# Optimization experiments

Measured on AMD Instinct MI355X. Metric: run time of the kernel, lower is better.

## Reference

```python
import jax, jax.numpy as jnp
import numpy as np

BSZ, T, D_IN, P, H, D_OUT = 8, 4096, 512, 256, 256, 512


def setup_inputs() -> dict:
    key = jax.random.key(0)
    ks = jax.random.split(key, 8)
    x_seq = jax.random.normal(ks[0], (BSZ, T, D_IN), dtype=jnp.float32)
    # stable diagonal transition: |a| < 1 so the 4096-step recurrence does not blow up
    a = jax.random.uniform(ks[1], (H,), minval=-0.99, maxval=0.99, dtype=jnp.float32)
    B = jax.random.normal(ks[2], (P, H), dtype=jnp.float32) * 0.05
    C = jax.random.normal(ks[3], (H, P), dtype=jnp.float32) * 0.05
    Wi = jax.random.normal(ks[4], (P, D_IN), dtype=jnp.float32) * 0.05
    bi = jax.random.normal(ks[5], (P,), dtype=jnp.float32) * 0.05
    Wo = jax.random.normal(ks[6], (D_OUT, P), dtype=jnp.float32) * 0.05
    bo = jax.random.normal(ks[7], (D_OUT,), dtype=jnp.float32) * 0.05
    return {"x_seq": x_seq, "a": a, "B": B, "C": C, "Wi": Wi, "bi": bi, "Wo": Wo, "bo": bo}


def reference(x_seq, a, B, C, Wi, bi, Wo, bo):
    # proj_in + relu (eqx.nn.Linear: y = W @ x + b), vmapped over batch and time
    x_proj = jax.nn.relu(jnp.einsum("btd,pd->btp", x_seq, Wi) + bi)  # [Bsz,T,P]
    # precompute driving input u_t = B^T x_t for every step
    u = jnp.einsum("btp,ph->bth", x_proj, B)  # [Bsz,T,H]
    u_t = jnp.swapaxes(u, 0, 1)  # [T,Bsz,H] (scan over time)

    def step(h, u_step):  # h: [Bsz,H]
        h = a * h + u_step
        return h, h

    h0 = jnp.zeros((x_seq.shape[0], a.shape[0]), dtype=x_seq.dtype)
    _, hs = jax.lax.scan(step, h0, u_t)  # hs: [T,Bsz,H]
    # y_t = C^T h_t, then proj_out
    y_seq = jnp.einsum("tbh,hp->btp", hs, C)  # [Bsz,T,P]
    y_out = jnp.einsum("btp,op->bto", y_seq, Wo) + bo  # [Bsz,T,D_out]
    return y_out
```

## Files before the change

kernel.cpp:

```cpp
#include <hip/hip_runtime.h>

#define BSZN 8
#define TT 4096
#define DIN 512
#define PP 256
#define HHH 256
#define DOUT 512
#define NROWS (BSZN * TT)
#define LCH 128
#define NC (TT / LCH)

typedef __attribute__((ext_vector_type(8))) short bf16x8;
typedef __attribute__((ext_vector_type(4))) float f32x4;

#define GLOBAL_AS __attribute__((address_space(1)))
#define LDS_AS __attribute__((address_space(3)))

static __device__ __forceinline__ void gld_lds16(const void* g, void* l) {
  __builtin_amdgcn_global_load_lds((const GLOBAL_AS unsigned int*)g,
                                   (LDS_AS unsigned int*)l, 16, 0, 0);
}

static __device__ __forceinline__ unsigned short f2bf(float x) {
  union { float f; unsigned u; } t{x};
  unsigned r = t.u + 0x7fffu + ((t.u >> 16) & 1u);
  return (unsigned short)(r >> 16);
}

__global__ __launch_bounds__(256) void gemm_cwt(
    const unsigned short* __restrict__ Ap, const unsigned short* __restrict__ Bp,
    unsigned short* __restrict__ Cp, int M, int N, int K) {
  __shared__ alignas(16) char smem[16384];
  char* As = smem;
  char* Bs = smem + 8192;
  const int tid = threadIdx.x, wave = tid >> 6, lane = tid & 63;
  const int m0 = blockIdx.x * 128, n0 = blockIdx.y * 128;
  const int wrow = (wave >> 1) * 64, wcol = (wave & 1) * 64;

  f32x4 acc[4][4];
#pragma unroll
  for (int i = 0; i < 4; ++i)
#pragma unroll
    for (int j = 0; j < 4; ++j) acc[i][j] = f32x4{0.f, 0.f, 0.f, 0.f};

  for (int k0 = 0; k0 < K; k0 += 32) {
#pragma unroll
    for (int it = 0; it < 2; ++it) {
      const int r = it * 64 + wave * 16 + (lane >> 2);
      const int cB = (lane & 3) * 16;
      gld_lds16((const char*)(Ap + (size_t)(m0 + r) * K + k0) + cB, As + r * 64 + cB);
      gld_lds16((const char*)(Bp + (size_t)(n0 + r) * K + k0) + cB, Bs + r * 64 + cB);
    }
    __syncthreads();
    bf16x8 af[4], bfv[4];
#pragma unroll
    for (int mi = 0; mi < 4; ++mi)
      af[mi] = *(const bf16x8*)(As + (wrow + mi * 16 + (lane & 15)) * 64 + (lane >> 4) * 16);
#pragma unroll
    for (int ni = 0; ni < 4; ++ni)
      bfv[ni] = *(const bf16x8*)(Bs + (wcol + ni * 16 + (lane & 15)) * 64 + (lane >> 4) * 16);
#pragma unroll
    for (int mi = 0; mi < 4; ++mi)
#pragma unroll
      for (int ni = 0; ni < 4; ++ni)
        acc[mi][ni] = __builtin_amdgcn_mfma_f32_16x16x32_bf16(af[mi], bfv[ni], acc[mi][ni], 0, 0, 0);
    __syncthreads();
  }
#pragma unroll
  for (int mi = 0; mi < 4; ++mi)
#pragma unroll
    for (int ni = 0; ni < 4; ++ni)
#pragma unroll
      for (int reg = 0; reg < 4; ++reg) {
        const int row = m0 + wrow + mi * 16 + (lane >> 4) * 4 + reg;
        const int col = n0 + wcol + ni * 16 + (lane & 15);
        Cp[(size_t)row * N + col] = f2bf(acc[mi][ni][reg]);
      }
}

__global__ __launch_bounds__(256) void conv_w_k(
    const float* __restrict__ Wi, const float* __restrict__ Wo,
    const float* __restrict__ Cm, const float* __restrict__ Bm,
    unsigned short* __restrict__ Wi_b, unsigned short* __restrict__ Wo_b,
    unsigned short* __restrict__ C_b, unsigned short* __restrict__ B_bT,
    int* __restrict__ flag_g) {
  const int b = blockIdx.x;
  const int tid = threadIdx.x;
  if (b < 320) {
    const float* src;
    unsigned short* dst;
    int idx;
    if (b < 128) { src = Wi; dst = Wi_b; idx = b * 1024 + tid * 4; }
    else if (b < 256) { src = Wo; dst = Wo_b; idx = (b - 128) * 1024 + tid * 4; }
    else { src = Cm; dst = C_b; idx = (b - 256) * 1024 + tid * 4; }
    const float4 v = *(const float4*)(src + idx);
    uint2 w;
    w.x = (unsigned)f2bf(v.x) | ((unsigned)f2bf(v.y) << 16);
    w.y = (unsigned)f2bf(v.z) | ((unsigned)f2bf(v.w) << 16);
    *(uint2*)(dst + idx) = w;
  } else if (b < 576) {
    const int p = b - 320;
    const int h = tid;
    B_bT[(size_t)h * PP + p] = f2bf(Bm[(size_t)p * HHH + h]);
  } else {
    flag_g[tid] = 0;
  }
}

__global__ __launch_bounds__(256, 1) void s4_mega(
    const float* __restrict__ x, const float* __restrict__ a,
    const unsigned short* __restrict__ Wi_b, const float* __restrict__ bi,
    const unsigned short* __restrict__ B_bT,
    const unsigned short* __restrict__ CWT_b, const float* __restrict__ bo,
    float* __restrict__ out, float* __restrict__ carry_g,
    int* __restrict__ flag_g) {
  __shared__ alignas(16) char smem[65536];
  char* As = smem;
  char* Bs = smem + 8192;

  const int tid = threadIdx.x, wave = tid >> 6, lane = tid & 63;
  const int bc = blockIdx.x, b = bc >> 5, c = bc & 31;
  const size_t row0 = (size_t)bc * LCH;
  const int wrow = (wave >> 1) * 64;
  const int wcol = (wave & 1) * 128;
  const int l15 = lane & 15, q = lane >> 4;

  f32x4 acc[4][8];
#pragma unroll
  for (int i = 0; i < 4; ++i)
#pragma unroll
    for (int j = 0; j < 8; ++j) acc[i][j] = f32x4{0.f, 0.f, 0.f, 0.f};

  for (int k0 = 0; k0 < DIN; k0 += 32) {
#pragma unroll
    for (int it = 0; it < 4; ++it) {
      const int f = it * 256 + tid;
      const int r = f >> 3, ck = (f & 7) * 4;
      const float4 v = *(const float4*)(x + (row0 + r) * DIN + k0 + ck);
      uint2 w;
      w.x = (unsigned)f2bf(v.x) | ((unsigned)f2bf(v.y) << 16);
      w.y = (unsigned)f2bf(v.z) | ((unsigned)f2bf(v.w) << 16);
      *(uint2*)(As + r * 64 + ck * 2) = w;
    }
#pragma unroll
    for (int it = 0; it < 4; ++it) {
      const int R0 = it * 64 + wave * 16;
      const int row = R0 + (lane >> 2), cB = (lane & 3) * 16;
      gld_lds16((const char*)(Wi_b + (size_t)row * DIN + k0) + cB, Bs + row * 64 + cB);
    }
    __syncthreads();
    bf16x8 af[4], bfv[8];
#pragma unroll
    for (int mi = 0; mi < 4; ++mi)
      af[mi] = *(const bf16x8*)(As + (wrow + mi * 16 + l15) * 64 + q * 16);
#pragma unroll
    for (int ni = 0; ni < 8; ++ni)
      bfv[ni] = *(const bf16x8*)(Bs + (wcol + ni * 16 + l15) * 64 + q * 16);
#pragma unroll
    for (int mi = 0; mi < 4; ++mi)
#pragma unroll
      for (int ni = 0; ni < 8; ++ni)
        acc[mi][ni] = __builtin_amdgcn_mfma_f32_16x16x32_bf16(af[mi], bfv[ni], acc[mi][ni], 0, 0, 0);
    __syncthreads();
  }

  unsigned short* xp = (unsigned short*)smem;
#pragma unroll
  for (int mi = 0; mi < 4; ++mi)
#pragma unroll
    for (int ni = 0; ni < 8; ++ni) {
      const int col = wcol + ni * 16 + l15;
      const float bb = bi[col];
#pragma unroll
      for (int reg = 0; reg < 4; ++reg) {
        const int row = wrow + mi * 16 + q * 4 + reg;
        float v = acc[mi][ni][reg] + bb;
        v = fmaxf(v, 0.f);
        xp[row * 256 + col] = f2bf(v);
      }
    }
  __syncthreads();

  f32x4 uacc[4][8];
#pragma unroll
  for (int i = 0; i < 4; ++i)
#pragma unroll
    for (int j = 0; j < 8; ++j) uacc[i][j] = f32x4{0.f, 0.f, 0.f, 0.f};
  for (int k0 = 0; k0 < PP; k0 += 32) {
    bf16x8 af[4], bfv[8];
#pragma unroll
    for (int mi = 0; mi < 4; ++mi)
      af[mi] = *(const bf16x8*)(xp + (wrow + mi * 16 + l15) * 256 + k0 + q * 8);
#pragma unroll
    for (int ni = 0; ni < 8; ++ni) {
      const int h = wcol + ni * 16 + l15;
      bfv[ni] = *(const bf16x8*)(B_bT + (size_t)h * PP + k0 + q * 8);
    }
#pragma unroll
    for (int mi = 0; mi < 4; ++mi)
#pragma unroll
      for (int ni = 0; ni < 8; ++ni)
        uacc[mi][ni] = __builtin_amdgcn_mfma_f32_16x16x32_bf16(af[mi], bfv[ni], uacc[mi][ni], 0, 0, 0);
  }
  __syncthreads();

  float carry0 = 0.f, carry1 = 0.f;
  float* uL = (float*)smem;
#pragma unroll
  for (int kh = 0; kh < 2; ++kh) {
    if ((wave & 1) == kh) {
#pragma unroll
      for (int mi = 0; mi < 4; ++mi)
#pragma unroll
        for (int ni = 0; ni < 8; ++ni) {
          const int colh = ni * 16 + l15;
#pragma unroll
          for (int reg = 0; reg < 4; ++reg) {
            const int row = wrow + mi * 16 + q * 4 + reg;
            uL[row * 128 + colh] = uacc[mi][ni][reg];
          }
        }
    }
    __syncthreads();
    if (tid < 128) {
      const float ah = a[kh * 128 + tid];
      float l = 0.f;
#pragma unroll 4
      for (int i = 0; i < LCH; ++i) {
        l = fmaf(ah, l, uL[i * 128 + tid]);
        uL[i * 128 + tid] = l;
      }
      if (kh == 0) carry0 = l; else carry1 = l;
    }
    __syncthreads();
    if ((wave & 1) == kh) {
#pragma unroll
      for (int mi = 0; mi < 4; ++mi)
#pragma unroll
        for (int ni = 0; ni < 8; ++ni) {
          const int colh = ni * 16 + l15;
#pragma unroll
          for (int reg = 0; reg < 4; ++reg) {
            const int row = wrow + mi * 16 + q * 4 + reg;
            uacc[mi][ni][reg] = uL[row * 128 + colh];
          }
        }
    }
    __syncthreads();
  }

  if (tid < 128) {
    __hip_atomic_store(&carry_g[(size_t)bc * HHH + tid], carry0,
                       __ATOMIC_RELAXED, __HIP_MEMORY_SCOPE_AGENT);
    __hip_atomic_store(&carry_g[(size_t)bc * HHH + 128 + tid], carry1,
                       __ATOMIC_RELAXED, __HIP_MEMORY_SCOPE_AGENT);
  }
  __syncthreads();
  if (tid == 0) {
    __threadfence();
    __hip_atomic_store(&flag_g[bc], 1, __ATOMIC_RELEASE, __HIP_MEMORY_SCOPE_AGENT);
  }
  if (tid < c) {
    while (__hip_atomic_load(&flag_g[b * NC + tid], __ATOMIC_ACQUIRE,
                             __HIP_MEMORY_SCOPE_AGENT) == 0)
      __builtin_amdgcn_s_sleep(8);
  }
  __syncthreads();
  float P = 0.f;
  {
    const float ah = a[tid];
    float aL = ah;
#pragma unroll
    for (int j = 0; j < 7; ++j) aL *= aL;
    for (int j = 0; j < c; ++j)
      P = fmaf(aL, P,
               __hip_atomic_load(&carry_g[((size_t)b * NC + j) * HHH + tid],
                                 __ATOMIC_RELAXED, __HIP_MEMORY_SCOPE_AGENT));
  }
  float* PL = (float*)smem;
  PL[tid] = P;
  __syncthreads();
#pragma unroll
  for (int ni = 0; ni < 8; ++ni) {
    const int col = wcol + ni * 16 + l15;
    const float Pc = PL[col];
    const float A = a[col];
    const float A2 = A * A, A4 = A2 * A2, A8 = A4 * A4, A16 = A8 * A8;
    const float A32 = A16 * A16, A64 = A32 * A32;
    float base = A * ((q & 1) ? A4 : 1.f) * ((q & 2) ? A8 : 1.f) *
                 (wrow ? A64 : 1.f);
    float rowf = base;
#pragma unroll
    for (int mi = 0; mi < 4; ++mi) {
      float fr = rowf;
#pragma unroll
      for (int reg = 0; reg < 4; ++reg) {
        uacc[mi][ni][reg] = fmaf(fr, Pc, uacc[mi][ni][reg]);
        fr *= A;
      }
      rowf *= A16;
    }
  }
  __syncthreads();

  unsigned short* hsL = (unsigned short*)smem;
#pragma unroll
  for (int mi = 0; mi < 4; ++mi)
#pragma unroll
    for (int ni = 0; ni < 8; ++ni) {
      const int col = wcol + ni * 16 + l15;
#pragma unroll
      for (int reg = 0; reg < 4; ++reg) {
        const int row = wrow + mi * 16 + q * 4 + reg;
        hsL[row * 256 + col] = f2bf(uacc[mi][ni][reg]);
      }
    }
  __syncthreads();

  for (int n = 0; n < 4; ++n) {
    f32x4 oacc[4][4];
#pragma unroll
    for (int i = 0; i < 4; ++i)
#pragma unroll
      for (int j = 0; j < 4; ++j) oacc[i][j] = f32x4{0.f, 0.f, 0.f, 0.f};
    const int ocol0 = n * 128 + (wave & 1) * 64;
    for (int k0 = 0; k0 < HHH; k0 += 32) {
      bf16x8 af[4], bfv[4];
#pragma unroll
      for (int mi = 0; mi < 4; ++mi)
        af[mi] = *(const bf16x8*)(hsL + (wrow + mi * 16 + l15) * 256 + k0 + q * 8);
#pragma unroll
      for (int ni = 0; ni < 4; ++ni) {
        const int o = ocol0 + ni * 16 + l15;
        bfv[ni] = *(const bf16x8*)(CWT_b + (size_t)o * HHH + k0 + q * 8);
      }
#pragma unroll
      for (int mi = 0; mi < 4; ++mi)
#pragma unroll
        for (int ni = 0; ni < 4; ++ni)
          oacc[mi][ni] = __builtin_amdgcn_mfma_f32_16x16x32_bf16(af[mi], bfv[ni], oacc[mi][ni], 0, 0, 0);
    }
#pragma unroll
    for (int ni = 0; ni < 4; ++ni) {
      const int o = ocol0 + ni * 16 + l15;
      const float bb = bo[o];
#pragma unroll
      for (int mi = 0; mi < 4; ++mi)
#pragma unroll
        for (int reg = 0; reg < 4; ++reg) {
          const int row = wrow + mi * 16 + q * 4 + reg;
          out[(row0 + row) * DOUT + o] = oacc[mi][ni][reg] + bb;
        }
    }
  }
}

extern "C" void kernel_launch(void* const* d_in, const int* in_sizes, int n_in,
                              void* d_out, int out_size, void* d_ws,
                              size_t ws_size, hipStream_t stream) {
  const float* x  = (const float*)d_in[0];
  const float* a  = (const float*)d_in[1];
  const float* Bm = (const float*)d_in[2];
  const float* Cm = (const float*)d_in[3];
  const float* Wi = (const float*)d_in[4];
  const float* bi = (const float*)d_in[5];
  const float* Wo = (const float*)d_in[6];
  const float* bo = (const float*)d_in[7];
  float* out = (float*)d_out;

  char* ws = (char*)d_ws;
  unsigned short* Wi_b  = (unsigned short*)ws; ws += (size_t)PP * DIN * 2;
  unsigned short* Wo_b  = (unsigned short*)ws; ws += (size_t)DOUT * PP * 2;
  unsigned short* C_b   = (unsigned short*)ws; ws += (size_t)HHH * PP * 2;
  unsigned short* B_bT  = (unsigned short*)ws; ws += (size_t)HHH * PP * 2;
  unsigned short* CWT_b = (unsigned short*)ws; ws += (size_t)DOUT * HHH * 2;
  float* carry_g = (float*)ws; ws += (size_t)BSZN * NC * HHH * 4;
  int* flag_g = (int*)ws;

  conv_w_k<<<577, 256, 0, stream>>>(Wi, Wo, Cm, Bm, Wi_b, Wo_b, C_b, B_bT, flag_g);
  gemm_cwt<<<dim3(DOUT / 128, HHH / 128), 256, 0, stream>>>(Wo_b, C_b, CWT_b,
                                                            DOUT, HHH, PP);
  s4_mega<<<BSZN * NC, 256, 0, stream>>>(x, a, Wi_b, bi, B_bT, CWT_b, bo, out,
                                         carry_g, flag_g);
}
```

Measured before the change: 196.3 us.

## Halve chunk length, do in-register scan, merge prep kernels, raise occupancy

```diff
diff --git a/kernel.cpp b/kernel.cpp
--- a/kernel.cpp
+++ b/kernel.cpp
@@ -6,9 +6,10 @@
 #define PP 256
 #define HHH 256
 #define DOUT 512
-#define NROWS (BSZN * TT)
-#define LCH 128
-#define NC (TT / LCH)
+#define LCH 64
+#define NCH (TT / LCH)
+#define NBLK (BSZN * NCH)
+#define XPS 264
 
 typedef __attribute__((ext_vector_type(8))) short bf16x8;
 typedef __attribute__((ext_vector_type(4))) float f32x4;
@@ -27,233 +28,236 @@
   return (unsigned short)(r >> 16);
 }
 
-__global__ __launch_bounds__(256) void gemm_cwt(
-    const unsigned short* __restrict__ Ap, const unsigned short* __restrict__ Bp,
-    unsigned short* __restrict__ Cp, int M, int N, int K) {
-  __shared__ alignas(16) char smem[16384];
-  char* As = smem;
-  char* Bs = smem + 8192;
-  const int tid = threadIdx.x, wave = tid >> 6, lane = tid & 63;
-  const int m0 = blockIdx.x * 128, n0 = blockIdx.y * 128;
-  const int wrow = (wave >> 1) * 64, wcol = (wave & 1) * 64;
-
-  f32x4 acc[4][4];
-#pragma unroll
-  for (int i = 0; i < 4; ++i)
-#pragma unroll
-    for (int j = 0; j < 4; ++j) acc[i][j] = f32x4{0.f, 0.f, 0.f, 0.f};
-
-  for (int k0 = 0; k0 < K; k0 += 32) {
-#pragma unroll
-    for (int it = 0; it < 2; ++it) {
-      const int r = it * 64 + wave * 16 + (lane >> 2);
-      const int cB = (lane & 3) * 16;
-      gld_lds16((const char*)(Ap + (size_t)(m0 + r) * K + k0) + cB, As + r * 64 + cB);
-      gld_lds16((const char*)(Bp + (size_t)(n0 + r) * K + k0) + cB, Bs + r * 64 + cB);
-    }
-    __syncthreads();
-    bf16x8 af[4], bfv[4];
-#pragma unroll
-    for (int mi = 0; mi < 4; ++mi)
-      af[mi] = *(const bf16x8*)(As + (wrow + mi * 16 + (lane & 15)) * 64 + (lane >> 4) * 16);
-#pragma unroll
-    for (int ni = 0; ni < 4; ++ni)
-      bfv[ni] = *(const bf16x8*)(Bs + (wcol + ni * 16 + (lane & 15)) * 64 + (lane >> 4) * 16);
-#pragma unroll
-    for (int mi = 0; mi < 4; ++mi)
-#pragma unroll
-      for (int ni = 0; ni < 4; ++ni)
-        acc[mi][ni] = __builtin_amdgcn_mfma_f32_16x16x32_bf16(af[mi], bfv[ni], acc[mi][ni], 0, 0, 0);
-    __syncthreads();
-  }
-#pragma unroll
-  for (int mi = 0; mi < 4; ++mi)
-#pragma unroll
-    for (int ni = 0; ni < 4; ++ni)
-#pragma unroll
-      for (int reg = 0; reg < 4; ++reg) {
-        const int row = m0 + wrow + mi * 16 + (lane >> 4) * 4 + reg;
-        const int col = n0 + wcol + ni * 16 + (lane & 15);
-        Cp[(size_t)row * N + col] = f2bf(acc[mi][ni][reg]);
-      }
-}
-
-__global__ __launch_bounds__(256) void conv_w_k(
+static __device__ __forceinline__ float ld_carry(const float* p) {
+  return __hip_atomic_load(p, __ATOMIC_RELAXED, __HIP_MEMORY_SCOPE_AGENT);
+}
+
+__global__ __launch_bounds__(256) void prep_k(
     const float* __restrict__ Wi, const float* __restrict__ Wo,
     const float* __restrict__ Cm, const float* __restrict__ Bm,
-    unsigned short* __restrict__ Wi_b, unsigned short* __restrict__ Wo_b,
-    unsigned short* __restrict__ C_b, unsigned short* __restrict__ B_bT,
-    int* __restrict__ flag_g) {
-  const int b = blockIdx.x;
-  const int tid = threadIdx.x;
-  if (b < 320) {
-    const float* src;
-    unsigned short* dst;
-    int idx;
-    if (b < 128) { src = Wi; dst = Wi_b; idx = b * 1024 + tid * 4; }
-    else if (b < 256) { src = Wo; dst = Wo_b; idx = (b - 128) * 1024 + tid * 4; }
-    else { src = Cm; dst = C_b; idx = (b - 256) * 1024 + tid * 4; }
-    const float4 v = *(const float4*)(src + idx);
+    unsigned short* __restrict__ Wi_b, unsigned short* __restrict__ B_bT,
+    unsigned short* __restrict__ CWT_b, int* __restrict__ flag_g) {
+  __shared__ alignas(16) char smem[16384];
+  const int b = blockIdx.x, tid = threadIdx.x;
+  if (b < 128) {
+    const int idx = b * 1024 + tid * 4;
+    const float4 v = *(const float4*)(Wi + idx);
     uint2 w;
     w.x = (unsigned)f2bf(v.x) | ((unsigned)f2bf(v.y) << 16);
     w.y = (unsigned)f2bf(v.z) | ((unsigned)f2bf(v.w) << 16);
-    *(uint2*)(dst + idx) = w;
-  } else if (b < 576) {
-    const int p = b - 320;
-    const int h = tid;
-    B_bT[(size_t)h * PP + p] = f2bf(Bm[(size_t)p * HHH + h]);
+    *(uint2*)(Wi_b + idx) = w;
+  } else if (b < 384) {
+    const int p = b - 128;
+    B_bT[(size_t)tid * PP + p] = f2bf(Bm[(size_t)p * HHH + tid]);
+  } else if (b == 384) {
+    flag_g[tid] = 0;
+    flag_g[tid + 256] = 0;
   } else {
-    flag_g[tid] = 0;
-  }
-}
-
-__global__ __launch_bounds__(256, 1) void s4_mega(
+    const int t = b - 385;
+    const int m0 = (t >> 1) * 128, n0 = (t & 1) * 128;
+    char* As = smem;
+    char* Bs = smem + 8192;
+    const int wave = tid >> 6, lane = tid & 63;
+    const int l15 = lane & 15, q = lane >> 4;
+    const int wrow = (wave >> 1) * 64, wcol = (wave & 1) * 64;
+    f32x4 acc[4][4];
+#pragma unroll
+    for (int i = 0; i < 4; ++i)
+#pragma unroll
+      for (int j = 0; j < 4; ++j) acc[i][j] = f32x4{0.f, 0.f, 0.f, 0.f};
+    for (int k0 = 0; k0 < PP; k0 += 32) {
+#pragma unroll
+      for (int it = 0; it < 4; ++it) {
+        const int f = it * 256 + tid;
+        const int r = f >> 3, ck = (f & 7) * 4;
+        const float4 v = *(const float4*)(Wo + (size_t)(m0 + r) * PP + k0 + ck);
+        uint2 w;
+        w.x = (unsigned)f2bf(v.x) | ((unsigned)f2bf(v.y) << 16);
+        w.y = (unsigned)f2bf(v.z) | ((unsigned)f2bf(v.w) << 16);
+        *(uint2*)(As + r * 64 + ck * 2) = w;
+      }
+#pragma unroll
+      for (int it = 0; it < 4; ++it) {
+        const int f = it * 256 + tid;
+        const int r = f >> 3, ck = (f & 7) * 4;
+        const float4 v = *(const float4*)(Cm + (size_t)(n0 + r) * PP + k0 + ck);
+        uint2 w;
+        w.x = (unsigned)f2bf(v.x) | ((unsigned)f2bf(v.y) << 16);
+        w.y = (unsigned)f2bf(v.z) | ((unsigned)f2bf(v.w) << 16);
+        *(uint2*)(Bs + r * 64 + ck * 2) = w;
+      }
+      __syncthreads();
+      bf16x8 af[4], bfv[4];
+#pragma unroll
+      for (int mi = 0; mi < 4; ++mi)
+        af[mi] = *(const bf16x8*)(As + (wrow + mi * 16 + l15) * 64 + q * 16);
+#pragma unroll
+      for (int ni = 0; ni < 4; ++ni)
+        bfv[ni] = *(const bf16x8*)(Bs + (wcol + ni * 16 + l15) * 64 + q * 16);
+#pragma unroll
+      for (int mi = 0; mi < 4; ++mi)
+#pragma unroll
+        for (int ni = 0; ni < 4; ++ni)
+          acc[mi][ni] = __builtin_amdgcn_mfma_f32_16x16x32_bf16(
+              af[mi], bfv[ni], acc[mi][ni], 0, 0, 0);
+      __syncthreads();
+    }
+#pragma unroll
+    for (int mi = 0; mi < 4; ++mi)
+#pragma unroll
+      for (int ni = 0; ni < 4; ++ni)
+#pragma unroll
+        for (int reg = 0; reg < 4; ++reg) {
+          const int row = m0 + wrow + mi * 16 + q * 4 + reg;
+          const int col = n0 + wcol + ni * 16 + l15;
+          CWT_b[(size_t)row * HHH + col] = f2bf(acc[mi][ni][reg]);
+        }
+  }
+}
+
+__global__ __launch_bounds__(256, 2) void s4_mega(
     const float* __restrict__ x, const float* __restrict__ a,
     const unsigned short* __restrict__ Wi_b, const float* __restrict__ bi,
     const unsigned short* __restrict__ B_bT,
     const unsigned short* __restrict__ CWT_b, const float* __restrict__ bo,
     float* __restrict__ out, float* __restrict__ carry_g,
     int* __restrict__ flag_g) {
-  __shared__ alignas(16) char smem[65536];
+  __shared__ alignas(16) char smem[64 * XPS * 2 + 1024];
   char* As = smem;
-  char* Bs = smem + 8192;
+  char* Bs = smem + 4096;
+  float* PL = (float*)(smem + 64 * XPS * 2);
 
   const int tid = threadIdx.x, wave = tid >> 6, lane = tid & 63;
-  const int bc = blockIdx.x, b = bc >> 5, c = bc & 31;
+  const int l15 = lane & 15, q = lane >> 4;
+  const int bc = blockIdx.x, b = bc >> 6, c = bc & 63;
   const size_t row0 = (size_t)bc * LCH;
-  const int wrow = (wave >> 1) * 64;
-  const int wcol = (wave & 1) * 128;
-  const int l15 = lane & 15, q = lane >> 4;
-
-  f32x4 acc[4][8];
+  const int wc = wave * 64;
+
+  f32x4 acc[4][4];
 #pragma unroll
   for (int i = 0; i < 4; ++i)
 #pragma unroll
-    for (int j = 0; j < 8; ++j) acc[i][j] = f32x4{0.f, 0.f, 0.f, 0.f};
-
+    for (int j = 0; j < 4; ++j) acc[i][j] = f32x4{0.f, 0.f, 0.f, 0.f};
+
+  float4 xv0, xv1;
+  {
+    const int f0 = tid, f1 = tid + 256;
+    xv0 = *(const float4*)(x + (row0 + (f0 >> 3)) * DIN + (f0 & 7) * 4);
+    xv1 = *(const float4*)(x + (row0 + (f1 >> 3)) * DIN + (f1 & 7) * 4);
+  }
   for (int k0 = 0; k0 < DIN; k0 += 32) {
+    {
+      const int f0 = tid, f1 = tid + 256;
+      uint2 w;
+      w.x = (unsigned)f2bf(xv0.x) | ((unsigned)f2bf(xv0.y) << 16);
+      w.y = (unsigned)f2bf(xv0.z) | ((unsigned)f2bf(xv0.w) << 16);
+      *(uint2*)(As + (f0 >> 3) * 64 + (f0 & 7) * 8) = w;
+      w.x = (unsigned)f2bf(xv1.x) | ((unsigned)f2bf(xv1.y) << 16);
+      w.y = (unsigned)f2bf(xv1.z) | ((unsigned)f2bf(xv1.w) << 16);
+      *(uint2*)(As + (f1 >> 3) * 64 + (f1 & 7) * 8) = w;
+    }
 #pragma unroll
     for (int it = 0; it < 4; ++it) {
-      const int f = it * 256 + tid;
-      const int r = f >> 3, ck = (f & 7) * 4;
-      const float4 v = *(const float4*)(x + (row0 + r) * DIN + k0 + ck);
-      uint2 w;
-      w.x = (unsigned)f2bf(v.x) | ((unsigned)f2bf(v.y) << 16);
-      w.y = (unsigned)f2bf(v.z) | ((unsigned)f2bf(v.w) << 16);
-      *(uint2*)(As + r * 64 + ck * 2) = w;
-    }
-#pragma unroll
-    for (int it = 0; it < 4; ++it) {
-      const int R0 = it * 64 + wave * 16;
-      const int row = R0 + (lane >> 2), cB = (lane & 3) * 16;
-      gld_lds16((const char*)(Wi_b + (size_t)row * DIN + k0) + cB, Bs + row * 64 + cB);
+      const int row = it * 64 + wave * 16 + (lane >> 2);
+      const int cB = (lane & 3) * 16;
+      gld_lds16((const char*)(Wi_b + (size_t)row * DIN + k0) + cB,
+                Bs + row * 64 + cB);
     }
     __syncthreads();
-    bf16x8 af[4], bfv[8];
-#pragma unroll
-    for (int mi = 0; mi < 4; ++mi)
-      af[mi] = *(const bf16x8*)(As + (wrow + mi * 16 + l15) * 64 + q * 16);
-#pragma unroll
-    for (int ni = 0; ni < 8; ++ni)
-      bfv[ni] = *(const bf16x8*)(Bs + (wcol + ni * 16 + l15) * 64 + q * 16);
-#pragma unroll
-    for (int mi = 0; mi < 4; ++mi)
-#pragma unroll
-      for (int ni = 0; ni < 8; ++ni)
-        acc[mi][ni] = __builtin_amdgcn_mfma_f32_16x16x32_bf16(af[mi], bfv[ni], acc[mi][ni], 0, 0, 0);
+    if (k0 + 32 < DIN) {
+      const int f0 = tid, f1 = tid + 256;
+      xv0 = *(const float4*)(x + (row0 + (f0 >> 3)) * DIN + k0 + 32 + (f0 & 7) * 4);
+      xv1 = *(const float4*)(x + (row0 + (f1 >> 3)) * DIN + k0 + 32 + (f1 & 7) * 4);
+    }
+    bf16x8 af[4], bfv[4];
+#pragma unroll
+    for (int mi = 0; mi < 4; ++mi)
+      af[mi] = *(const bf16x8*)(As + (mi * 16 + l15) * 64 + q * 16);
+#pragma unroll
+    for (int ni = 0; ni < 4; ++ni)
+      bfv[ni] = *(const bf16x8*)(Bs + (wc + ni * 16 + l15) * 64 + q * 16);
+#pragma unroll
+    for (int mi = 0; mi < 4; ++mi)
+#pragma unroll
+      for (int ni = 0; ni < 4; ++ni)
+        acc[mi][ni] = __builtin_amdgcn_mfma_f32_16x16x32_bf16(
+            af[mi], bfv[ni], acc[mi][ni], 0, 0, 0);
     __syncthreads();
   }
 
   unsigned short* xp = (unsigned short*)smem;
 #pragma unroll
-  for (int mi = 0; mi < 4; ++mi)
-#pragma unroll
-    for (int ni = 0; ni < 8; ++ni) {
-      const int col = wcol + ni * 16 + l15;
-      const float bb = bi[col];
+  for (int ni = 0; ni < 4; ++ni) {
+    const int col = wc + ni * 16 + l15;
+    const float bb = bi[col];
+#pragma unroll
+    for (int mi = 0; mi < 4; ++mi)
 #pragma unroll
       for (int reg = 0; reg < 4; ++reg) {
-        const int row = wrow + mi * 16 + q * 4 + reg;
-        float v = acc[mi][ni][reg] + bb;
-        v = fmaxf(v, 0.f);
-        xp[row * 256 + col] = f2bf(v);
+        const int row = mi * 16 + q * 4 + reg;
+        xp[row * XPS + col] = f2bf(fmaxf(acc[ni < 2 ? mi : mi][ni][reg] + bb, 0.f));
       }
-    }
-  __syncthreads();
-
-  f32x4 uacc[4][8];
+  }
+  __syncthreads();
+
 #pragma unroll
   for (int i = 0; i < 4; ++i)
 #pragma unroll
-    for (int j = 0; j < 8; ++j) uacc[i][j] = f32x4{0.f, 0.f, 0.f, 0.f};
+    for (int j = 0; j < 4; ++j) acc[i][j] = f32x4{0.f, 0.f, 0.f, 0.f};
   for (int k0 = 0; k0 < PP; k0 += 32) {
-    bf16x8 af[4], bfv[8];
-#pragma unroll
-    for (int mi = 0; mi < 4; ++mi)
-      af[mi] = *(const bf16x8*)(xp + (wrow + mi * 16 + l15) * 256 + k0 + q * 8);
-#pragma unroll
-    for (int ni = 0; ni < 8; ++ni) {
-      const int h = wcol + ni * 16 + l15;
-      bfv[ni] = *(const bf16x8*)(B_bT + (size_t)h * PP + k0 + q * 8);
-    }
-#pragma unroll
-    for (int mi = 0; mi < 4; ++mi)
-#pragma unroll
-      for (int ni = 0; ni < 8; ++ni)
-        uacc[mi][ni] = __builtin_amdgcn_mfma_f32_16x16x32_bf16(af[mi], bfv[ni], uacc[mi][ni], 0, 0, 0);
-  }
-  __syncthreads();
-
-  float carry0 = 0.f, carry1 = 0.f;
-  float* uL = (float*)smem;
-#pragma unroll
-  for (int kh = 0; kh < 2; ++kh) {
-    if ((wave & 1) == kh) {
-#pragma unroll
-      for (int mi = 0; mi < 4; ++mi)
-#pragma unroll
-        for (int ni = 0; ni < 8; ++ni) {
-          const int colh = ni * 16 + l15;
-#pragma unroll
-          for (int reg = 0; reg < 4; ++reg) {
-            const int row = wrow + mi * 16 + q * 4 + reg;
-            uL[row * 128 + colh] = uacc[mi][ni][reg];
-          }
-        }
-    }
-    __syncthreads();
-    if (tid < 128) {
-      const float ah = a[kh * 128 + tid];
-      float l = 0.f;
-#pragma unroll 4
-      for (int i = 0; i < LCH; ++i) {
-        l = fmaf(ah, l, uL[i * 128 + tid]);
-        uL[i * 128 + tid] = l;
-      }
-      if (kh == 0) carry0 = l; else carry1 = l;
-    }
-    __syncthreads();
-    if ((wave & 1) == kh) {
-#pragma unroll
-      for (int mi = 0; mi < 4; ++mi)
-#pragma unroll
-        for (int ni = 0; ni < 8; ++ni) {
-          const int colh = ni * 16 + l15;
-#pragma unroll
-          for (int reg = 0; reg < 4; ++reg) {
-            const int row = wrow + mi * 16 + q * 4 + reg;
-            uacc[mi][ni][reg] = uL[row * 128 + colh];
-          }
-        }
-    }
-    __syncthreads();
-  }
-
-  if (tid < 128) {
-    __hip_atomic_store(&carry_g[(size_t)bc * HHH + tid], carry0,
-                       __ATOMIC_RELAXED, __HIP_MEMORY_SCOPE_AGENT);
-    __hip_atomic_store(&carry_g[(size_t)bc * HHH + 128 + tid], carry1,
-                       __ATOMIC_RELAXED, __HIP_MEMORY_SCOPE_AGENT);
+    bf16x8 af[4], bfv[4];
+#pragma unroll
+    for (int mi = 0; mi < 4; ++mi)
+      af[mi] = *(const bf16x8*)(xp + (mi * 16 + l15) * XPS + k0 + q * 8);
+#pragma unroll
+    for (int ni = 0; ni < 4; ++ni)
+      bfv[ni] = *(const bf16x8*)(B_bT + (size_t)(wc + ni * 16 + l15) * PP + k0 + q * 8);
+#pragma unroll
+    for (int mi = 0; mi < 4; ++mi)
+#pragma unroll
+      for (int ni = 0; ni < 4; ++ni)
+        acc[mi][ni] = __builtin_amdgcn_mfma_f32_16x16x32_bf16(
+            af[mi], bfv[ni], acc[mi][ni], 0, 0, 0);
+  }
+
+  float aC[4], Wz[4];
+#pragma unroll
+  for (int ni = 0; ni < 4; ++ni) aC[ni] = a[wc + ni * 16 + l15];
+#pragma unroll
+  for (int ni = 0; ni < 4; ++ni) {
+    const float A = aC[ni];
+    const float A2 = A * A, A4 = A2 * A2, A8 = A4 * A4, A16 = A8 * A8;
+    const float A4q = ((q & 1) ? A4 : 1.f) * ((q & 2) ? A8 : 1.f);
+    float W = 0.f;
+#pragma unroll
+    for (int mi = 0; mi < 4; ++mi) {
+      f32x4 v = acc[mi][ni];
+      v.y = fmaf(A, v.x, v.y);
+      v.z = fmaf(A, v.y, v.z);
+      v.w = fmaf(A, v.z, v.w);
+      const float E = v.w;
+      const float E0 = __shfl(E, l15, 64);
+      const float E1 = __shfl(E, l15 + 16, 64);
+      const float E2 = __shfl(E, l15 + 32, 64);
+      const float E3 = __shfl(E, l15 + 48, 64);
+      const float s1 = E0, s2 = fmaf(A4, s1, E1), s3 = fmaf(A4, s2, E2);
+      const float s4 = fmaf(A4, s3, E3);
+      const float Sq = (q == 0) ? 0.f : (q == 1) ? s1 : (q == 2) ? s2 : s3;
+      const float sin_ = fmaf(A4q, W, Sq);
+      v.x = fmaf(A, sin_, v.x);
+      v.y = fmaf(A2, sin_, v.y);
+      v.z = fmaf(A2 * A, sin_, v.z);
+      v.w = fmaf(A4, sin_, v.w);
+      acc[mi][ni] = v;
+      W = fmaf(A16, W, s4);
+    }
+    Wz[ni] = W;
+  }
+  if (q == 0) {
+#pragma unroll
+    for (int ni = 0; ni < 4; ++ni)
+      __hip_atomic_store(&carry_g[(size_t)bc * HHH + wc + ni * 16 + l15],
+                         Wz[ni], __ATOMIC_RELAXED, __HIP_MEMORY_SCOPE_AGENT);
   }
   __syncthreads();
   if (tid == 0) {
@@ -261,95 +265,97 @@
     __hip_atomic_store(&flag_g[bc], 1, __ATOMIC_RELEASE, __HIP_MEMORY_SCOPE_AGENT);
   }
   if (tid < c) {
-    while (__hip_atomic_load(&flag_g[b * NC + tid], __ATOMIC_ACQUIRE,
+    while (__hip_atomic_load(&flag_g[b * NCH + tid], __ATOMIC_ACQUIRE,
                              __HIP_MEMORY_SCOPE_AGENT) == 0)
       __builtin_amdgcn_s_sleep(8);
   }
   __syncthreads();
-  float P = 0.f;
   {
-    const float ah = a[tid];
-    float aL = ah;
-#pragma unroll
-    for (int j = 0; j < 7; ++j) aL *= aL;
-    for (int j = 0; j < c; ++j)
-      P = fmaf(aL, P,
-               __hip_atomic_load(&carry_g[((size_t)b * NC + j) * HHH + tid],
-                                 __ATOMIC_RELAXED, __HIP_MEMORY_SCOPE_AGENT));
-  }
-  float* PL = (float*)smem;
-  PL[tid] = P;
-  __syncthreads();
-#pragma unroll
-  for (int ni = 0; ni < 8; ++ni) {
-    const int col = wcol + ni * 16 + l15;
-    const float Pc = PL[col];
-    const float A = a[col];
+    const int colp = tid;
+    const float A = a[colp];
+    float t1 = A;
+#pragma unroll
+    for (int j = 0; j < 6; ++j) t1 *= t1;
+    const float A64 = t1, A128 = A64 * A64, A256 = A128 * A128;
+    const float* cg = carry_g + (size_t)b * NCH * HHH + colp;
+    float P = 0.f;
+    int j = 0;
+    for (; j + 4 <= c; j += 4) {
+      const float c0 = ld_carry(cg + (size_t)j * HHH);
+      const float c1 = ld_carry(cg + (size_t)(j + 1) * HHH);
+      const float c2 = ld_carry(cg + (size_t)(j + 2) * HHH);
+      const float c3 = ld_carry(cg + (size_t)(j + 3) * HHH);
+      P = fmaf(A256, P, fmaf(A64, fmaf(A64, fmaf(A64, c0, c1), c2), c3));
+    }
+    for (; j < c; ++j) P = fmaf(A64, P, ld_carry(cg + (size_t)j * HHH));
+    PL[colp] = P;
+  }
+  __syncthreads();
+#pragma unroll
+  for (int ni = 0; ni < 4; ++ni) {
+    const float A = aC[ni];
     const float A2 = A * A, A4 = A2 * A2, A8 = A4 * A4, A16 = A8 * A8;
-    const float A32 = A16 * A16, A64 = A32 * A32;
-    float base = A * ((q & 1) ? A4 : 1.f) * ((q & 2) ? A8 : 1.f) *
-                 (wrow ? A64 : 1.f);
-    float rowf = base;
+    const float A4q = ((q & 1) ? A4 : 1.f) * ((q & 2) ? A8 : 1.f);
+    const float P = PL[wc + ni * 16 + l15];
+    float fm = A4q * A * P;
 #pragma unroll
     for (int mi = 0; mi < 4; ++mi) {
-      float fr = rowf;
-#pragma unroll
-      for (int reg = 0; reg < 4; ++reg) {
-        uacc[mi][ni][reg] = fmaf(fr, Pc, uacc[mi][ni][reg]);
-        fr *= A;
-      }
-      rowf *= A16;
+      f32x4 v = acc[mi][ni];
+      v.x += fm;
+      v.y = fmaf(A, fm, v.y);
+      v.z = fmaf(A2, fm, v.z);
+      v.w = fmaf(A2 * A, fm, v.w);
+      acc[mi][ni] = v;
+      fm *= A16;
     }
   }
   __syncthreads();
 
   unsigned short* hsL = (unsigned short*)smem;
 #pragma unroll
-  for (int mi = 0; mi < 4; ++mi)
-#pragma unroll
-    for (int ni = 0; ni < 8; ++ni) {
-      const int col = wcol + ni * 16 + l15;
-#pragma unroll
-      for (int reg = 0; reg < 4; ++reg) {
-        const int row = wrow + mi * 16 + q * 4 + reg;
-        hsL[row * 256 + col] = f2bf(uacc[mi][ni][reg]);
-      }
-    }
-  __syncthreads();
-
-  for (int n = 0; n < 4; ++n) {
+  for (int ni = 0; ni < 4; ++ni) {
+    const int col = wc + ni * 16 + l15;
+#pragma unroll
+    for (int mi = 0; mi < 4; ++mi)
+#pragma unroll
+      for (int reg = 0; reg < 4; ++reg)
+        hsL[(mi * 16 + q * 4 + reg) * XPS + col] = f2bf(acc[mi][ni][reg]);
+  }
+  __syncthreads();
+
+#pragma unroll
+  for (int g = 0; g < 2; ++g) {
+    const int gc0 = wave * 128 + g * 64;
     f32x4 oacc[4][4];
 #pragma unroll
     for (int i = 0; i < 4; ++i)
 #pragma unroll
       for (int j = 0; j < 4; ++j) oacc[i][j] = f32x4{0.f, 0.f, 0.f, 0.f};
-    const int ocol0 = n * 128 + (wave & 1) * 64;
     for (int k0 = 0; k0 < HHH; k0 += 32) {
       bf16x8 af[4], bfv[4];
 #pragma unroll
       for (int mi = 0; mi < 4; ++mi)
-        af[mi] = *(const bf16x8*)(hsL + (wrow + mi * 16 + l15) * 256 + k0 + q * 8);
-#pragma unroll
-      for (int ni = 0; ni < 4; ++ni) {
-        const int o = ocol0 + ni * 16 + l15;
-        bfv[ni] = *(const bf16x8*)(CWT_b + (size_t)o * HHH + k0 + q * 8);
-      }
+        af[mi] = *(const bf16x8*)(hsL + (mi * 16 + l15) * XPS + k0 + q * 8);
+#pragma unroll
+      for (int ni = 0; ni < 4; ++ni)
+        bfv[ni] = *(const bf16x8*)(CWT_b + (size_t)(gc0 + ni * 16 + l15) * HHH + k0 + q * 8);
 #pragma unroll
       for (int mi = 0; mi < 4; ++mi)
 #pragma unroll
         for (int ni = 0; ni < 4; ++ni)
-          oacc[mi][ni] = __builtin_amdgcn_mfma_f32_16x16x32_bf16(af[mi], bfv[ni], oacc[mi][ni], 0, 0, 0);
+          oacc[mi][ni] = __builtin_amdgcn_mfma_f32_16x16x32_bf16(
+              af[mi], bfv[ni], oacc[mi][ni], 0, 0, 0);
     }
 #pragma unroll
     for (int ni = 0; ni < 4; ++ni) {
-      const int o = ocol0 + ni * 16 + l15;
-      const float bb = bo[o];
+      const int ocol = gc0 + ni * 16 + l15;
+      const float bb = bo[ocol];
 #pragma unroll
       for (int mi = 0; mi < 4; ++mi)
 #pragma unroll
         for (int reg = 0; reg < 4; ++reg) {
-          const int row = wrow + mi * 16 + q * 4 + reg;
-          out[(row0 + row) * DOUT + o] = oacc[mi][ni][reg] + bb;
+          const int row = mi * 16 + q * 4 + reg;
+          out[(row0 + row) * DOUT + ocol] = oacc[mi][ni][reg] + bb;
         }
     }
   }
@@ -370,16 +376,12 @@
 
   char* ws = (char*)d_ws;
   unsigned short* Wi_b  = (unsigned short*)ws; ws += (size_t)PP * DIN * 2;
-  unsigned short* Wo_b  = (unsigned short*)ws; ws += (size_t)DOUT * PP * 2;
-  unsigned short* C_b   = (unsigned short*)ws; ws += (size_t)HHH * PP * 2;
   unsigned short* B_bT  = (unsigned short*)ws; ws += (size_t)HHH * PP * 2;
   unsigned short* CWT_b = (unsigned short*)ws; ws += (size_t)DOUT * HHH * 2;
-  float* carry_g = (float*)ws; ws += (size_t)BSZN * NC * HHH * 4;
+  float* carry_g = (float*)ws; ws += (size_t)NBLK * HHH * 4;
   int* flag_g = (int*)ws;
 
-  conv_w_k<<<577, 256, 0, stream>>>(Wi, Wo, Cm, Bm, Wi_b, Wo_b, C_b, B_bT, flag_g);
-  gemm_cwt<<<dim3(DOUT / 128, HHH / 128), 256, 0, stream>>>(Wo_b, C_b, CWT_b,
-                                                            DOUT, HHH, PP);
-  s4_mega<<<BSZN * NC, 256, 0, stream>>>(x, a, Wi_b, bi, B_bT, CWT_b, bo, out,
-                                         carry_g, flag_g);
-}
+  prep_k<<<393, 256, 0, stream>>>(Wi, Wo, Cm, Bm, Wi_b, B_bT, CWT_b, flag_g);
+  s4_mega<<<NBLK, 256, 0, stream>>>(x, a, Wi_b, bi, B_bT, CWT_b, bo, out,
+                                    carry_g, flag_g);
+}
```

New measurement: 194.3 us. No clear change (-1.0%).
